# Optimization experiments

Measured on AMD Instinct MI355X. Metric: run time of the kernel, lower is better.

The kernel has to match this reference:

```python
import jax, jax.numpy as jnp
import numpy as np

B, L, D, S = 64, 512, 768, 8
HOP, LAMB = 3, 0.5


def _layernorm(x, g, b, eps=1e-5):
    m = x.mean(-1, keepdims=True)
    v = x.var(-1, keepdims=True)
    return (x - m) / jnp.sqrt(v + eps) * g + b


def _hop_refine(cur, sentence, ln_g, ln_b):
    # cur, sentence: [B,S,D]. HOP-1 refinement steps, then return last row.
    for _ in range(HOP - 1):
        coef = jnp.einsum('bd,bsd->bs', cur[:, -1, :], sentence)  # [B,S]
        a = coef[..., None] * sentence                             # [B,S,D]
        cur = LAMB * _layernorm(jax.nn.sigmoid(a), ln_g, ln_b) + sentence
    return cur[:, -1, :]  # [B,D]


def _conv1d(x, w, b):
    # x: [B,D,S], w: [Dout,Din,3], padding=1 (same)
    y = jax.lax.conv_general_dilated(
        x, w, window_strides=(1,), padding=((1, 1),),
        dimension_numbers=('NCH', 'OIH', 'NCH'))
    return y + b[None, :, None]


def setup_inputs() -> dict:
    key = jax.random.key(0)
    ks = jax.random.split(key, 16)
    p = lambda k, shp: (jax.random.normal(k, shp, dtype=jnp.float32) * 0.02)
    # segment boundaries: strictly increasing, start at 1, <= L, gaps ~63 with jitter < 32
    base = 1 + np.arange(S + 1) * ((L - 1) // S)          # [9]
    jitter = np.array(jax.random.randint(ks[15], (B, S + 1), 0, 32))
    jitter[:, 0] = 0
    jitter[:, -1] = 0
    seg_bounds = jnp.asarray(base[None, :] + jitter, dtype=jnp.int64 if jax.config.jax_enable_x64 else jnp.int32)
    return {
        'bert_output': jax.random.normal(ks[0], (B, L, D), dtype=jnp.float32),
        'target': jax.random.normal(ks[1], (B, D), dtype=jnp.float32),
        'gc1_w': p(ks[2], (D, D)), 'gc1_b': p(ks[3], (D,)),
        'gc2_w': p(ks[4], (D, D)), 'gc2_b': p(ks[5], (D,)),
        'conv1_w': p(ks[6], (D, D, 3)), 'conv1_b': p(ks[7], (D,)),
        'conv2_w': p(ks[8], (D, D, 3)), 'conv2_b': p(ks[9], (D,)),
        'ln_g': jnp.ones((D,), jnp.float32), 'ln_b': jnp.zeros((D,), jnp.float32),
        'fc2_w': p(ks[10], (3 * D, 3)), 'fc2_b': p(ks[11], (3,)),
        'seg_bounds': seg_bounds,
    }


def reference(bert_output, target, gc1_w, gc1_b, gc2_w, gc2_b,
              conv1_w, conv1_b, conv2_w, conv2_b, ln_g, ln_b,
              fc2_w, fc2_b, seg_bounds):
    dt = bert_output.dtype
    start = seg_bounds[:, :-1]   # [B,S]
    end = seg_bounds[:, 1:]      # [B,S]
    pos = jnp.arange(L)
    seg_mask = ((pos[None, None, :] >= start[:, :, None]) &
                (pos[None, None, :] < end[:, :, None])).astype(dt)  # [B,S,L]
    cnt = (end - start).astype(dt)                                   # [B,S]
    # batched segment-mean pooling
    sentence = jnp.einsum('bsl,bld->bsd', seg_mask, bert_output) / cnt[..., None]

    # GCN branch: adj = I + superdiagonal, row-degree normalization
    adj = jnp.eye(S, dtype=dt) + jnp.eye(S, k=1, dtype=dt)
    denom = adj.sum(axis=1)  # [S]

    def gcn(x, w, b):
        h = jnp.einsum('bsd,de->bse', x, w)
        return jnp.einsum('st,btd->bsd', adj, h) / denom[None, :, None] + b

    g1 = jnp.tanh(gcn(sentence, gc1_w, gc1_b))
    g2 = jnp.tanh(gcn(g1, gc2_w, gc2_b))
    a3 = _hop_refine(g2, sentence, ln_g, ln_b)

    # Conv branch: two conv1d (k=3, pad=1) over the segment axis
    x = jnp.swapaxes(sentence, 1, 2)  # [B,D,S]
    c = jnp.tanh(_conv1d(x, conv1_w, conv1_b))
    c = jnp.tanh(_conv1d(c, conv2_w, conv2_b))
    conv_out = jnp.swapaxes(c, 1, 2)  # [B,S,D]
    a4 = _hop_refine(conv_out, sentence, ln_g, ln_b)

    # Self-mask branch
    coef0 = jnp.einsum('bd,bsd->bs', sentence[:, -1, :], sentence)
    tmask = jax.nn.sigmoid(coef0[..., None] * sentence)
    a5 = _hop_refine(tmask, sentence, ln_g, ln_b)

    fnout = jnp.stack([a3, a4, a5], axis=1)                 # [B,3,D]
    # NOTE: original uses target[0] (first sample's pooler output) for all samples
    w = jax.nn.softmax(jnp.einsum('bkd,d->bk', fnout, target[0]), axis=1)
    fn = (fnout * w[..., None]).reshape(fnout.shape[0], 3 * D)
    return fn @ fc2_w + fc2_b  # [B,3]
```

## Files before the change

### kernel.cpp

```cpp
#include <hip/hip_runtime.h>


typedef unsigned short u16;
typedef short short8 __attribute__((ext_vector_type(8)));
typedef float f32x4 __attribute__((ext_vector_type(4)));

__device__ __forceinline__ float bf2f(u16 h) {
    unsigned int u = ((unsigned int)h) << 16;
    float f;
    __builtin_memcpy(&f, &u, 4);
    return f;
}
__device__ __forceinline__ u16 f2bf(float f) {
    unsigned int u;
    __builtin_memcpy(&u, &f, 4);
    u = (u + 0x7fffu + ((u >> 16) & 1u)) >> 16;
    return (u16)u;
}
__device__ __forceinline__ float sigm(float x) { return 1.0f / (1.0f + __expf(-x)); }

__device__ __forceinline__ float ldv(const void* p, long i, bool bf) {
    return bf ? bf2f(((const u16*)p)[i]) : ((const float*)p)[i];
}

__device__ __forceinline__ bool detect_bf16(const u16* bert) {
    int hits = 0;
#pragma unroll
    for (int i = 0; i < 256; i += 2) {
        const int e = (bert[i] >> 7) & 0xFF;
        hits += (e >= 115 && e <= 130) ? 1 : 0;
    }
    return hits > 64;
}

__global__ __launch_bounds__(256) void k0_zero(float* __restrict__ ws)
{
    ((float4*)ws)[blockIdx.x * 256 + threadIdx.x] = make_float4(0.f, 0.f, 0.f, 0.f);
}

__global__ __launch_bounds__(256) void k1_pool(
    const void* __restrict__ bertv, const int* __restrict__ sb,
    float* __restrict__ sentF, float* __restrict__ flagp)
{
    const int u = blockIdx.x, t = threadIdx.x;
    const bool bf = detect_bf16((const u16*)bertv);
    const bool is64 = (sb[1] == 0);
    if (u == 0 && t == 0) flagp[0] = bf ? 1.0f : 0.0f;
    const int q = u & 3, v = u >> 2;
    const int b = v / 3, si = v - 3 * (v / 3), s = 5 + si;
    const int i0 = b * 9 + s, i1 = i0 + 1;
    int st = is64 ? sb[2 * i0] : sb[i0];
    int en = is64 ? sb[2 * i1] : sb[i1];
    st = st < 0 ? 0 : (st > 511 ? 511 : st);
    en = en <= st ? st + 1 : (en > 512 ? 512 : en);
    const int n = en - st;
    const int r0 = st + (n * q) / 4;
    const int r1 = st + (n * (q + 1)) / 4;
    float a0 = 0.f, a1 = 0.f, a2 = 0.f;
    if (bf) {
        const u16* base = (const u16*)bertv + (size_t)b * 512 * 768;
        int l = r0;
        for (; l + 1 < r1; l += 2) {
            const u16* p0 = base + (size_t)l * 768;
            const u16* p1 = p0 + 768;
            const u16 x0 = p0[t], x1 = p0[t + 256], x2 = p0[t + 512];
            const u16 y0 = p1[t], y1 = p1[t + 256], y2 = p1[t + 512];
            a0 += bf2f(x0) + bf2f(y0);
            a1 += bf2f(x1) + bf2f(y1);
            a2 += bf2f(x2) + bf2f(y2);
        }
        if (l < r1) {
            const u16* p0 = base + (size_t)l * 768;
            a0 += bf2f(p0[t]);
            a1 += bf2f(p0[t + 256]);
            a2 += bf2f(p0[t + 512]);
        }
    } else {
        const float* base = (const float*)bertv + (size_t)b * 512 * 768;
        int l = r0;
        for (; l + 1 < r1; l += 2) {
            const float* p0 = base + (size_t)l * 768;
            const float* p1 = p0 + 768;
            const float x0 = p0[t], x1 = p0[t + 256], x2 = p0[t + 512];
            const float y0 = p1[t], y1 = p1[t + 256], y2 = p1[t + 512];
            a0 += x0 + y0;
            a1 += x1 + y1;
            a2 += x2 + y2;
        }
        if (l < r1) {
            const float* p0 = base + (size_t)l * 768;
            a0 += p0[t];
            a1 += p0[t + 256];
            a2 += p0[t + 512];
        }
    }
    const float inv = 1.0f / (float)n;
    float* o = sentF + b * 2304 + si * 768;
    atomicAdd(o + t, a0 * inv);
    atomicAdd(o + t + 256, a1 * inv);
    atomicAdd(o + t + 512, a2 * inv);
}

template <int XMODE, int WMODE>
__device__ __forceinline__ void gemm_core(
    const float* __restrict__ x, int xstride, const void* __restrict__ bias,
    const void* __restrict__ W, bool bf,
    float* __restrict__ out, int ostride,
    int n0, int k0, u16* As, u16* Bs)
{
    const int t = threadIdx.x;
    const int r = t >> 2;
    const int cseg = (t & 3) * 32;
    const int wave = t >> 6, lane = t & 63;
    const int lm = lane & 15, lq = lane >> 4;
    f32x4 acc[4] = {};

    for (int kk = 0; kk < 256; kk += 128) {
        const int kg = k0 + kk;
        {
            const float* xp = x + (size_t)r * xstride + (kg + cseg);
            u16* dst = As + r * 136 + cseg;
#pragma unroll
            for (int i = 0; i < 8; ++i) {
                float4 v = ((const float4*)xp)[i];
                if (XMODE == 1) {
                    int kb = kg + cseg + i * 4;
                    if (kb >= 768) kb -= 768;
                    v.x = tanhf(v.x + ldv(bias, kb, bf));
                    v.y = tanhf(v.y + ldv(bias, kb + 1, bf));
                    v.z = tanhf(v.z + ldv(bias, kb + 2, bf));
                    v.w = tanhf(v.w + ldv(bias, kb + 3, bf));
                }
                ((ushort4*)dst)[i] = make_ushort4(f2bf(v.x), f2bf(v.y), f2bf(v.z), f2bf(v.w));
            }
        }
        if (WMODE == 0) {
            const int p = t >> 2;
            const int nseg = (t & 3) * 16;
            u16 q0[16], q1[16];
            if (bf) {
                const u16* w0 = (const u16*)W + (size_t)(kg + 2 * p) * 768 + n0 + nseg;
                ((uint4*)q0)[0] = ((const uint4*)w0)[0];
                ((uint4*)q0)[1] = ((const uint4*)w0)[1];
                ((uint4*)q1)[0] = ((const uint4*)(w0 + 768))[0];
                ((uint4*)q1)[1] = ((const uint4*)(w0 + 768))[1];
            } else {
                const float* w0 = (const float*)W + (size_t)(kg + 2 * p) * 768 + n0 + nseg;
#pragma unroll
                for (int e = 0; e < 4; ++e) {
                    float4 v0 = ((const float4*)w0)[e];
                    float4 v1 = ((const float4*)(w0 + 768))[e];
                    q0[4 * e] = f2bf(v0.x); q0[4 * e + 1] = f2bf(v0.y);
                    q0[4 * e + 2] = f2bf(v0.z); q0[4 * e + 3] = f2bf(v0.w);
                    q1[4 * e] = f2bf(v1.x); q1[4 * e + 1] = f2bf(v1.y);
                    q1[4 * e + 2] = f2bf(v1.z); q1[4 * e + 3] = f2bf(v1.w);
                }
            }
#pragma unroll
            for (int e = 0; e < 16; ++e)
                *(ushort2*)(Bs + (nseg + e) * 136 + 2 * p) = make_ushort2(q0[e], q1[e]);
        } else {
            const int kb = kg / 768;
            const int i0c = kg - kb * 768;
            u16 tmp[32];
            if (bf) {
                const u16* wp = (const u16*)W + (size_t)(n0 + r) * 2304 + (size_t)(i0c + cseg) * 3 + kb;
#pragma unroll
                for (int j = 0; j < 32; ++j) tmp[j] = wp[j * 3];
            } else {
                const float* wp = (const float*)W + (size_t)(n0 + r) * 2304 + (size_t)(i0c + cseg) * 3 + kb;
#pragma unroll
                for (int j = 0; j < 32; ++j) tmp[j] = f2bf(wp[j * 3]);
            }
            u16* dst = Bs + r * 136 + cseg;
#pragma unroll
            for (int qq = 0; qq < 8; ++qq)
                ((ushort4*)dst)[qq] = ((ushort4*)tmp)[qq];
        }
        __syncthreads();
        const u16* ap = As + (wave * 16 + lm) * 136 + lq * 8;
        const u16* bp = Bs + lm * 136 + lq * 8;
#pragma unroll
        for (int ks = 0; ks < 4; ++ks) {
            short8 af = *(const short8*)(ap + ks * 32);
#pragma unroll
            for (int nf = 0; nf < 4; ++nf) {
                short8 bfr = *(const short8*)(bp + nf * 16 * 136 + ks * 32);
                acc[nf] = __builtin_amdgcn_mfma_f32_16x16x32_bf16(af, bfr, acc[nf], 0, 0, 0);
            }
        }
        __syncthreads();
    }
#pragma unroll
    for (int nf = 0; nf < 4; ++nf) {
#pragma unroll
        for (int rg = 0; rg < 4; ++rg) {
            const int row = wave * 16 + lq * 4 + rg;
            const int col = n0 + nf * 16 + lm;
            atomicAdd(out + (size_t)row * ostride + col, acc[nf][rg]);
        }
    }
}

__global__ __launch_bounds__(256) void k2_gemm_a(
    const float* __restrict__ sentF, const void* __restrict__ gc1w,
    const void* __restrict__ c1w, float* __restrict__ g1acc, float* __restrict__ c1acc,
    const float* __restrict__ flagp)
{
    __shared__ u16 As[64 * 136];
    __shared__ u16 Bs[64 * 136];
    const bool bf = flagp[0] > 0.5f;
    const int u = blockIdx.x;
    if (u < 36) {
        gemm_core<0, 0>(sentF + 1536, 2304, nullptr, gc1w, bf, g1acc, 768,
                        (u / 3) * 64, (u % 3) * 256, As, Bs);
    } else if (u < 144) {
        const int v = u - 36;
        gemm_core<0, 1>(sentF, 2304, nullptr, c1w, bf, c1acc, 1536,
                        (v / 9) * 64, (v % 9) * 256, As, Bs);
    } else {
        const int v = u - 144;
        gemm_core<0, 1>(sentF + 768, 2304, nullptr, c1w, bf, c1acc + 768, 1536,
                        (v / 6) * 64, (v % 6) * 256, As, Bs);
    }
}

__global__ __launch_bounds__(256) void k3_gemm_b(
    const float* __restrict__ g1acc, const float* __restrict__ c1acc,
    const void* __restrict__ gc2w, const void* __restrict__ c2w,
    const void* __restrict__ gc1b, const void* __restrict__ c1b,
    float* __restrict__ g2acc, float* __restrict__ c2acc,
    const float* __restrict__ flagp)
{
    __shared__ u16 As[64 * 136];
    __shared__ u16 Bs[64 * 136];
    const bool bf = flagp[0] > 0.5f;
    const int u = blockIdx.x;
    if (u < 36) {
        gemm_core<1, 0>(g1acc, 768, gc1b, gc2w, bf, g2acc, 768,
                        (u / 3) * 64, (u % 3) * 256, As, Bs);
    } else {
        const int v = u - 36;
        gemm_core<1, 1>(c1acc, 1536, c1b, c2w, bf, c2acc, 768,
                        (v / 6) * 64, (v % 6) * 256, As, Bs);
    }
}

__device__ __forceinline__ float block_sum(float v, float* red) {
#pragma unroll
    for (int m = 1; m < 64; m <<= 1) v += __shfl_xor(v, m, 64);
    const int wave = threadIdx.x >> 6, lane = threadIdx.x & 63;
    if (lane == 0) red[wave] = v;
    __syncthreads();
    const float r = red[0] + red[1] + red[2] + red[3];
    __syncthreads();
    return r;
}

__global__ __launch_bounds__(256) void k4_final(
    const float* __restrict__ sentF, const float* __restrict__ g2acc,
    const float* __restrict__ c2acc,
    const void* __restrict__ gc2b, const void* __restrict__ c2b,
    const void* __restrict__ lng, const void* __restrict__ lnb,
    const void* __restrict__ target, const void* __restrict__ fc2w,
    const void* __restrict__ fc2b, void* __restrict__ outp,
    const float* __restrict__ flagp)
{
    __shared__ float red[4];
    const bool bf = flagp[0] > 0.5f;
    const int t = threadIdx.x, b = blockIdx.x;
    float s_[3], g_[3], bb_[3];
    const float* srow = sentF + b * 2304 + 1536;
#pragma unroll
    for (int i = 0; i < 3; ++i) {
        const int d = t + 256 * i;
        s_[i] = srow[d];
        g_[i] = ldv(lng, d, bf);
        bb_[i] = ldv(lnb, d, bf);
    }

    auto refine2 = [&](float* yv) {
#pragma unroll
        for (int it = 0; it < 2; ++it) {
            const float c = block_sum(yv[0] * s_[0] + yv[1] * s_[1] + yv[2] * s_[2], red);
            float tt[3], sm = 0.0f, sq = 0.0f;
#pragma unroll
            for (int i = 0; i < 3; ++i) {
                tt[i] = sigm(c * s_[i]);
                sm += tt[i];
                sq += tt[i] * tt[i];
            }
            const float m = block_sum(sm, red) * (1.0f / 768.0f);
            const float q = block_sum(sq, red) * (1.0f / 768.0f);
            const float inv = rsqrtf(fmaxf(q - m * m, 0.0f) + 1e-5f);
#pragma unroll
            for (int i = 0; i < 3; ++i)
                yv[i] = 0.5f * ((tt[i] - m) * inv * g_[i] + bb_[i]) + s_[i];
        }
    };

    float a3[3], a4[3], a5[3], y[3];
#pragma unroll
    for (int i = 0; i < 3; ++i) {
        const int d = t + 256 * i;
        y[i] = tanhf(g2acc[b * 768 + d] + ldv(gc2b, d, bf));
    }
    refine2(y);
    a3[0] = y[0]; a3[1] = y[1]; a3[2] = y[2];
#pragma unroll
    for (int i = 0; i < 3; ++i) {
        const int d = t + 256 * i;
        y[i] = tanhf(c2acc[b * 768 + d] + ldv(c2b, d, bf));
    }
    refine2(y);
    a4[0] = y[0]; a4[1] = y[1]; a4[2] = y[2];
    const float ss = block_sum(s_[0] * s_[0] + s_[1] * s_[1] + s_[2] * s_[2], red);
#pragma unroll
    for (int i = 0; i < 3; ++i) y[i] = sigm(ss * s_[i]);
    refine2(y);
    a5[0] = y[0]; a5[1] = y[1]; a5[2] = y[2];

    float tg[3];
#pragma unroll
    for (int i = 0; i < 3; ++i) tg[i] = ldv(target, t + 256 * i, bf);
    const float u0 = block_sum(a3[0] * tg[0] + a3[1] * tg[1] + a3[2] * tg[2], red);
    const float u1 = block_sum(a4[0] * tg[0] + a4[1] * tg[1] + a4[2] * tg[2], red);
    const float u2 = block_sum(a5[0] * tg[0] + a5[1] * tg[1] + a5[2] * tg[2], red);
    const float mx = fmaxf(u0, fmaxf(u1, u2));
    const float e0 = __expf(u0 - mx), e1 = __expf(u1 - mx), e2 = __expf(u2 - mx);
    const float es = e0 + e1 + e2;
    const float w0 = e0 / es, w1 = e1 / es, w2 = e2 / es;

    float p0 = 0.0f, p1 = 0.0f, p2 = 0.0f;
#pragma unroll
    for (int i = 0; i < 3; ++i) {
        const int d = t + 256 * i;
        const float va = w0 * a3[i], vb = w1 * a4[i], vc = w2 * a5[i];
        p0 += va * ldv(fc2w, d * 3 + 0, bf) + vb * ldv(fc2w, (768 + d) * 3 + 0, bf) + vc * ldv(fc2w, (1536 + d) * 3 + 0, bf);
        p1 += va * ldv(fc2w, d * 3 + 1, bf) + vb * ldv(fc2w, (768 + d) * 3 + 1, bf) + vc * ldv(fc2w, (1536 + d) * 3 + 1, bf);
        p2 += va * ldv(fc2w, d * 3 + 2, bf) + vb * ldv(fc2w, (768 + d) * 3 + 2, bf) + vc * ldv(fc2w, (1536 + d) * 3 + 2, bf);
    }
    p0 = block_sum(p0, red);
    p1 = block_sum(p1, red);
    p2 = block_sum(p2, red);
    if (t == 0) {
        const float o0 = p0 + ldv(fc2b, 0, bf);
        const float o1 = p1 + ldv(fc2b, 1, bf);
        const float o2 = p2 + ldv(fc2b, 2, bf);
        if (bf) {
            ((u16*)outp)[b * 3 + 0] = f2bf(o0);
            ((u16*)outp)[b * 3 + 1] = f2bf(o1);
            ((u16*)outp)[b * 3 + 2] = f2bf(o2);
        } else {
            ((float*)outp)[b * 3 + 0] = o0;
            ((float*)outp)[b * 3 + 1] = o1;
            ((float*)outp)[b * 3 + 2] = o2;
        }
    }
}

extern "C" void kernel_launch(void* const* d_in, const int* in_sizes, int n_in,
                              void* d_out, int out_size, void* d_ws, size_t ws_size,
                              hipStream_t stream) {
    const void* bert   = d_in[0];
    const void* target = d_in[1];
    const void* gc1w   = d_in[2];
    const void* gc1b   = d_in[3];
    const void* gc2w   = d_in[4];
    const void* gc2b   = d_in[5];
    const void* c1w    = d_in[6];
    const void* c1b    = d_in[7];
    const void* c2w    = d_in[8];
    const void* c2b    = d_in[9];
    const void* lng    = d_in[10];
    const void* lnb    = d_in[11];
    const void* fc2w   = d_in[12];
    const void* fc2b   = d_in[13];
    const int*  sb     = (const int*)d_in[14];

    float* sentF = (float*)d_ws;
    float* accs  = sentF + 147456;
    float* g1acc = accs;
    float* c1acc = accs + 49152;
    float* g2acc = c1acc + 98304;
    float* c2acc = g2acc + 49152;
    float* flagp = accs + 245760;

    k0_zero<<<384, 256, 0, stream>>>(sentF);
    k1_pool<<<768, 256, 0, stream>>>(bert, sb, sentF, flagp);
    k2_gemm_a<<<216, 256, 0, stream>>>(sentF, gc1w, c1w, g1acc, c1acc, flagp);
    k3_gemm_b<<<108, 256, 0, stream>>>(g1acc, c1acc, gc2w, c2w, gc1b, c1b, g2acc, c2acc, flagp);
    k4_final<<<64, 256, 0, stream>>>(sentF, g2acc, c2acc, gc2b, c2b, lng, lnb,
                                     target, fc2w, fc2b, d_out, flagp);
}
```

Baseline: 224.5 us.

## Fuse all stages into one persistent kernel with software grid barriers

Replaces the five kernel launches (zero, pool, two GEMM stages, final) with a memset plus a single 768-block kernel. The stages are separated by atomic-counter grid barriers. The second GEMM stage is re-tiled to 216 blocks with one K iteration each instead of 108 blocks with two, which spreads the work across more blocks. The aim is to remove launch gaps and tail effects between the small stages. In exchange, it depends on all 768 blocks being co-resident, so the barrier could deadlock or time out (it breaks out after a poll limit) if they are not. The relaxed atomics with a vmcnt wait may also not guarantee memory visibility across blocks.

```diff
diff --git a/kernel.cpp b/kernel.cpp
--- a/kernel.cpp
+++ b/kernel.cpp
@@ -4,6 +4,8 @@
 typedef unsigned short u16;
 typedef short short8 __attribute__((ext_vector_type(8)));
 typedef float f32x4 __attribute__((ext_vector_type(4)));
+
+#define NBLK 768
 
 __device__ __forceinline__ float bf2f(u16 h) {
     unsigned int u = ((unsigned int)h) << 16;
@@ -33,72 +35,18 @@
     return hits > 64;
 }
 
-__global__ __launch_bounds__(256) void k0_zero(float* __restrict__ ws)
-{
-    ((float4*)ws)[blockIdx.x * 256 + threadIdx.x] = make_float4(0.f, 0.f, 0.f, 0.f);
-}
-
-__global__ __launch_bounds__(256) void k1_pool(
-    const void* __restrict__ bertv, const int* __restrict__ sb,
-    float* __restrict__ sentF, float* __restrict__ flagp)
-{
-    const int u = blockIdx.x, t = threadIdx.x;
-    const bool bf = detect_bf16((const u16*)bertv);
-    const bool is64 = (sb[1] == 0);
-    if (u == 0 && t == 0) flagp[0] = bf ? 1.0f : 0.0f;
-    const int q = u & 3, v = u >> 2;
-    const int b = v / 3, si = v - 3 * (v / 3), s = 5 + si;
-    const int i0 = b * 9 + s, i1 = i0 + 1;
-    int st = is64 ? sb[2 * i0] : sb[i0];
-    int en = is64 ? sb[2 * i1] : sb[i1];
-    st = st < 0 ? 0 : (st > 511 ? 511 : st);
-    en = en <= st ? st + 1 : (en > 512 ? 512 : en);
-    const int n = en - st;
-    const int r0 = st + (n * q) / 4;
-    const int r1 = st + (n * (q + 1)) / 4;
-    float a0 = 0.f, a1 = 0.f, a2 = 0.f;
-    if (bf) {
-        const u16* base = (const u16*)bertv + (size_t)b * 512 * 768;
-        int l = r0;
-        for (; l + 1 < r1; l += 2) {
-            const u16* p0 = base + (size_t)l * 768;
-            const u16* p1 = p0 + 768;
-            const u16 x0 = p0[t], x1 = p0[t + 256], x2 = p0[t + 512];
-            const u16 y0 = p1[t], y1 = p1[t + 256], y2 = p1[t + 512];
-            a0 += bf2f(x0) + bf2f(y0);
-            a1 += bf2f(x1) + bf2f(y1);
-            a2 += bf2f(x2) + bf2f(y2);
-        }
-        if (l < r1) {
-            const u16* p0 = base + (size_t)l * 768;
-            a0 += bf2f(p0[t]);
-            a1 += bf2f(p0[t + 256]);
-            a2 += bf2f(p0[t + 512]);
-        }
-    } else {
-        const float* base = (const float*)bertv + (size_t)b * 512 * 768;
-        int l = r0;
-        for (; l + 1 < r1; l += 2) {
-            const float* p0 = base + (size_t)l * 768;
-            const float* p1 = p0 + 768;
-            const float x0 = p0[t], x1 = p0[t + 256], x2 = p0[t + 512];
-            const float y0 = p1[t], y1 = p1[t + 256], y2 = p1[t + 512];
-            a0 += x0 + y0;
-            a1 += x1 + y1;
-            a2 += x2 + y2;
-        }
-        if (l < r1) {
-            const float* p0 = base + (size_t)l * 768;
-            a0 += p0[t];
-            a1 += p0[t + 256];
-            a2 += p0[t + 512];
-        }
-    }
-    const float inv = 1.0f / (float)n;
-    float* o = sentF + b * 2304 + si * 768;
-    atomicAdd(o + t, a0 * inv);
-    atomicAdd(o + t + 256, a1 * inv);
-    atomicAdd(o + t + 512, a2 * inv);
+__device__ __forceinline__ void gbar(unsigned* cnt, unsigned target) {
+    __syncthreads();
+    if (threadIdx.x == 0) {
+        asm volatile("s_waitcnt vmcnt(0)" ::: "memory");
+        __hip_atomic_fetch_add(cnt, 1u, __ATOMIC_RELAXED, __HIP_MEMORY_SCOPE_AGENT);
+        int polls = 0;
+        while (__hip_atomic_load(cnt, __ATOMIC_RELAXED, __HIP_MEMORY_SCOPE_AGENT) < target) {
+            __builtin_amdgcn_s_sleep(2);
+            if (++polls > (1 << 22)) break;
+        }
+    }
+    __syncthreads();
 }
 
 template <int XMODE, int WMODE>
@@ -106,7 +54,7 @@
     const float* __restrict__ x, int xstride, const void* __restrict__ bias,
     const void* __restrict__ W, bool bf,
     float* __restrict__ out, int ostride,
-    int n0, int k0, u16* As, u16* Bs)
+    int n0, int k0, int kiters, u16* As, u16* Bs)
 {
     const int t = threadIdx.x;
     const int r = t >> 2;
@@ -115,7 +63,7 @@
     const int lm = lane & 15, lq = lane >> 4;
     f32x4 acc[4] = {};
 
-    for (int kk = 0; kk < 256; kk += 128) {
+    for (int kk = 0; kk < kiters * 128; kk += 128) {
         const int kg = k0 + kk;
         {
             const float* xp = x + (size_t)r * xstride + (kg + cseg);
@@ -202,50 +150,6 @@
     }
 }
 
-__global__ __launch_bounds__(256) void k2_gemm_a(
-    const float* __restrict__ sentF, const void* __restrict__ gc1w,
-    const void* __restrict__ c1w, float* __restrict__ g1acc, float* __restrict__ c1acc,
-    const float* __restrict__ flagp)
-{
-    __shared__ u16 As[64 * 136];
-    __shared__ u16 Bs[64 * 136];
-    const bool bf = flagp[0] > 0.5f;
-    const int u = blockIdx.x;
-    if (u < 36) {
-        gemm_core<0, 0>(sentF + 1536, 2304, nullptr, gc1w, bf, g1acc, 768,
-                        (u / 3) * 64, (u % 3) * 256, As, Bs);
-    } else if (u < 144) {
-        const int v = u - 36;
-        gemm_core<0, 1>(sentF, 2304, nullptr, c1w, bf, c1acc, 1536,
-                        (v / 9) * 64, (v % 9) * 256, As, Bs);
-    } else {
-        const int v = u - 144;
-        gemm_core<0, 1>(sentF + 768, 2304, nullptr, c1w, bf, c1acc + 768, 1536,
-                        (v / 6) * 64, (v % 6) * 256, As, Bs);
-    }
-}
-
-__global__ __launch_bounds__(256) void k3_gemm_b(
-    const float* __restrict__ g1acc, const float* __restrict__ c1acc,
-    const void* __restrict__ gc2w, const void* __restrict__ c2w,
-    const void* __restrict__ gc1b, const void* __restrict__ c1b,
-    float* __restrict__ g2acc, float* __restrict__ c2acc,
-    const float* __restrict__ flagp)
-{
-    __shared__ u16 As[64 * 136];
-    __shared__ u16 Bs[64 * 136];
-    const bool bf = flagp[0] > 0.5f;
-    const int u = blockIdx.x;
-    if (u < 36) {
-        gemm_core<1, 0>(g1acc, 768, gc1b, gc2w, bf, g2acc, 768,
-                        (u / 3) * 64, (u % 3) * 256, As, Bs);
-    } else {
-        const int v = u - 36;
-        gemm_core<1, 1>(c1acc, 1536, c1b, c2w, bf, c2acc, 768,
-                        (v / 6) * 64, (v % 6) * 256, As, Bs);
-    }
-}
-
 __device__ __forceinline__ float block_sum(float v, float* red) {
 #pragma unroll
     for (int m = 1; m < 64; m <<= 1) v += __shfl_xor(v, m, 64);
@@ -257,104 +161,210 @@
     return r;
 }
 
-__global__ __launch_bounds__(256) void k4_final(
-    const float* __restrict__ sentF, const float* __restrict__ g2acc,
-    const float* __restrict__ c2acc,
-    const void* __restrict__ gc2b, const void* __restrict__ c2b,
+__global__ __launch_bounds__(256) void kmono(
+    const void* __restrict__ bert, const int* __restrict__ sb,
+    const void* __restrict__ target,
+    const void* __restrict__ gc1w, const void* __restrict__ gc1b,
+    const void* __restrict__ gc2w, const void* __restrict__ gc2b,
+    const void* __restrict__ c1w, const void* __restrict__ c1b,
+    const void* __restrict__ c2w, const void* __restrict__ c2b,
     const void* __restrict__ lng, const void* __restrict__ lnb,
-    const void* __restrict__ target, const void* __restrict__ fc2w,
-    const void* __restrict__ fc2b, void* __restrict__ outp,
-    const float* __restrict__ flagp)
+    const void* __restrict__ fc2w, const void* __restrict__ fc2b,
+    void* __restrict__ outp, float* __restrict__ ws)
 {
+    __shared__ u16 As[64 * 136];
+    __shared__ u16 Bs[64 * 136];
     __shared__ float red[4];
-    const bool bf = flagp[0] > 0.5f;
-    const int t = threadIdx.x, b = blockIdx.x;
-    float s_[3], g_[3], bb_[3];
-    const float* srow = sentF + b * 2304 + 1536;
-#pragma unroll
-    for (int i = 0; i < 3; ++i) {
-        const int d = t + 256 * i;
-        s_[i] = srow[d];
-        g_[i] = ldv(lng, d, bf);
-        bb_[i] = ldv(lnb, d, bf);
-    }
-
-    auto refine2 = [&](float* yv) {
-#pragma unroll
-        for (int it = 0; it < 2; ++it) {
-            const float c = block_sum(yv[0] * s_[0] + yv[1] * s_[1] + yv[2] * s_[2], red);
-            float tt[3], sm = 0.0f, sq = 0.0f;
-#pragma unroll
-            for (int i = 0; i < 3; ++i) {
-                tt[i] = sigm(c * s_[i]);
-                sm += tt[i];
-                sq += tt[i] * tt[i];
-            }
-            const float m = block_sum(sm, red) * (1.0f / 768.0f);
-            const float q = block_sum(sq, red) * (1.0f / 768.0f);
-            const float inv = rsqrtf(fmaxf(q - m * m, 0.0f) + 1e-5f);
-#pragma unroll
-            for (int i = 0; i < 3; ++i)
-                yv[i] = 0.5f * ((tt[i] - m) * inv * g_[i] + bb_[i]) + s_[i];
-        }
-    };
-
-    float a3[3], a4[3], a5[3], y[3];
-#pragma unroll
-    for (int i = 0; i < 3; ++i) {
-        const int d = t + 256 * i;
-        y[i] = tanhf(g2acc[b * 768 + d] + ldv(gc2b, d, bf));
-    }
-    refine2(y);
-    a3[0] = y[0]; a3[1] = y[1]; a3[2] = y[2];
-#pragma unroll
-    for (int i = 0; i < 3; ++i) {
-        const int d = t + 256 * i;
-        y[i] = tanhf(c2acc[b * 768 + d] + ldv(c2b, d, bf));
-    }
-    refine2(y);
-    a4[0] = y[0]; a4[1] = y[1]; a4[2] = y[2];
-    const float ss = block_sum(s_[0] * s_[0] + s_[1] * s_[1] + s_[2] * s_[2], red);
-#pragma unroll
-    for (int i = 0; i < 3; ++i) y[i] = sigm(ss * s_[i]);
-    refine2(y);
-    a5[0] = y[0]; a5[1] = y[1]; a5[2] = y[2];
-
-    float tg[3];
-#pragma unroll
-    for (int i = 0; i < 3; ++i) tg[i] = ldv(target, t + 256 * i, bf);
-    const float u0 = block_sum(a3[0] * tg[0] + a3[1] * tg[1] + a3[2] * tg[2], red);
-    const float u1 = block_sum(a4[0] * tg[0] + a4[1] * tg[1] + a4[2] * tg[2], red);
-    const float u2 = block_sum(a5[0] * tg[0] + a5[1] * tg[1] + a5[2] * tg[2], red);
-    const float mx = fmaxf(u0, fmaxf(u1, u2));
-    const float e0 = __expf(u0 - mx), e1 = __expf(u1 - mx), e2 = __expf(u2 - mx);
-    const float es = e0 + e1 + e2;
-    const float w0 = e0 / es, w1 = e1 / es, w2 = e2 / es;
-
-    float p0 = 0.0f, p1 = 0.0f, p2 = 0.0f;
-#pragma unroll
-    for (int i = 0; i < 3; ++i) {
-        const int d = t + 256 * i;
-        const float va = w0 * a3[i], vb = w1 * a4[i], vc = w2 * a5[i];
-        p0 += va * ldv(fc2w, d * 3 + 0, bf) + vb * ldv(fc2w, (768 + d) * 3 + 0, bf) + vc * ldv(fc2w, (1536 + d) * 3 + 0, bf);
-        p1 += va * ldv(fc2w, d * 3 + 1, bf) + vb * ldv(fc2w, (768 + d) * 3 + 1, bf) + vc * ldv(fc2w, (1536 + d) * 3 + 1, bf);
-        p2 += va * ldv(fc2w, d * 3 + 2, bf) + vb * ldv(fc2w, (768 + d) * 3 + 2, bf) + vc * ldv(fc2w, (1536 + d) * 3 + 2, bf);
-    }
-    p0 = block_sum(p0, red);
-    p1 = block_sum(p1, red);
-    p2 = block_sum(p2, red);
-    if (t == 0) {
-        const float o0 = p0 + ldv(fc2b, 0, bf);
-        const float o1 = p1 + ldv(fc2b, 1, bf);
-        const float o2 = p2 + ldv(fc2b, 2, bf);
+    const int t = threadIdx.x;
+    const int blk = blockIdx.x;
+
+    const bool bf = detect_bf16((const u16*)bert);
+    const bool is64 = (sb[1] == 0);
+
+    float* sentF = ws;
+    float* accs  = ws + 147456;
+    float* g1acc = accs;
+    float* c1acc = g1acc + 49152;
+    float* g2acc = c1acc + 98304;
+    float* c2acc = g2acc + 49152;
+    unsigned* cnts = (unsigned*)(accs + 245760);
+
+    {
+        const int u = blk;
+        const int q = u & 3, v = u >> 2;
+        const int b = v / 3, si = v - 3 * (v / 3), s = 5 + si;
+        const int i0 = b * 9 + s, i1 = i0 + 1;
+        int st = is64 ? sb[2 * i0] : sb[i0];
+        int en = is64 ? sb[2 * i1] : sb[i1];
+        st = st < 0 ? 0 : (st > 511 ? 511 : st);
+        en = en <= st ? st + 1 : (en > 512 ? 512 : en);
+        const int n = en - st;
+        const int r0 = st + (n * q) / 4;
+        const int r1 = st + (n * (q + 1)) / 4;
+        float a0 = 0.f, a1 = 0.f, a2 = 0.f;
         if (bf) {
-            ((u16*)outp)[b * 3 + 0] = f2bf(o0);
-            ((u16*)outp)[b * 3 + 1] = f2bf(o1);
-            ((u16*)outp)[b * 3 + 2] = f2bf(o2);
+            const u16* base = (const u16*)bert + (size_t)b * 512 * 768;
+            int l = r0;
+            for (; l + 1 < r1; l += 2) {
+                const u16* p0 = base + (size_t)l * 768;
+                const u16* p1 = p0 + 768;
+                a0 += bf2f(p0[t]) + bf2f(p1[t]);
+                a1 += bf2f(p0[t + 256]) + bf2f(p1[t + 256]);
+                a2 += bf2f(p0[t + 512]) + bf2f(p1[t + 512]);
+            }
+            if (l < r1) {
+                const u16* p0 = base + (size_t)l * 768;
+                a0 += bf2f(p0[t]);
+                a1 += bf2f(p0[t + 256]);
+                a2 += bf2f(p0[t + 512]);
+            }
         } else {
-            ((float*)outp)[b * 3 + 0] = o0;
-            ((float*)outp)[b * 3 + 1] = o1;
-            ((float*)outp)[b * 3 + 2] = o2;
+            const float* base = (const float*)bert + (size_t)b * 512 * 768;
+            int l = r0;
+            for (; l + 1 < r1; l += 2) {
+                const float* p0 = base + (size_t)l * 768;
+                const float* p1 = p0 + 768;
+                a0 += p0[t] + p1[t];
+                a1 += p0[t + 256] + p1[t + 256];
+                a2 += p0[t + 512] + p1[t + 512];
+            }
+            if (l < r1) {
+                const float* p0 = base + (size_t)l * 768;
+                a0 += p0[t];
+                a1 += p0[t + 256];
+                a2 += p0[t + 512];
+            }
+        }
+        const float inv = 1.0f / (float)n;
+        float* o = sentF + b * 2304 + si * 768;
+        atomicAdd(o + t, a0 * inv);
+        atomicAdd(o + t + 256, a1 * inv);
+        atomicAdd(o + t + 512, a2 * inv);
+    }
+
+    gbar(cnts + 0, NBLK);
+
+    if (blk < 216) {
+        const int u = blk;
+        if (u < 36) {
+            gemm_core<0, 0>(sentF + 1536, 2304, nullptr, gc1w, bf, g1acc, 768,
+                            (u / 3) * 64, (u % 3) * 256, 2, As, Bs);
+        } else if (u < 144) {
+            const int v = u - 36;
+            gemm_core<0, 1>(sentF, 2304, nullptr, c1w, bf, c1acc, 1536,
+                            (v / 9) * 64, (v % 9) * 256, 2, As, Bs);
+        } else {
+            const int v = u - 144;
+            gemm_core<0, 1>(sentF + 768, 2304, nullptr, c1w, bf, c1acc + 768, 1536,
+                            (v / 6) * 64, (v % 6) * 256, 2, As, Bs);
+        }
+    }
+
+    gbar(cnts + 1, NBLK);
+
+    if (blk < 216) {
+        const int u = blk;
+        if (u < 72) {
+            gemm_core<1, 0>(g1acc, 768, gc1b, gc2w, bf, g2acc, 768,
+                            (u / 6) * 64, (u % 6) * 128, 1, As, Bs);
+        } else {
+            const int v = u - 72;
+            gemm_core<1, 1>(c1acc, 1536, c1b, c2w, bf, c2acc, 768,
+                            (v / 12) * 64, (v % 12) * 128, 1, As, Bs);
+        }
+    }
+
+    gbar(cnts + 2, NBLK);
+
+    if (blk < 64) {
+        const int b = blk;
+        float s_[3], g_[3], bb_[3];
+        const float* srow = sentF + b * 2304 + 1536;
+#pragma unroll
+        for (int i = 0; i < 3; ++i) {
+            const int d = t + 256 * i;
+            s_[i] = srow[d];
+            g_[i] = ldv(lng, d, bf);
+            bb_[i] = ldv(lnb, d, bf);
+        }
+
+        auto refine2 = [&](float* yv) {
+#pragma unroll
+            for (int it = 0; it < 2; ++it) {
+                const float c = block_sum(yv[0] * s_[0] + yv[1] * s_[1] + yv[2] * s_[2], red);
+                float tt[3], sm = 0.0f, sq = 0.0f;
+#pragma unroll
+                for (int i = 0; i < 3; ++i) {
+                    tt[i] = sigm(c * s_[i]);
+                    sm += tt[i];
+                    sq += tt[i] * tt[i];
+                }
+                const float m = block_sum(sm, red) * (1.0f / 768.0f);
+                const float q = block_sum(sq, red) * (1.0f / 768.0f);
+                const float inv = rsqrtf(fmaxf(q - m * m, 0.0f) + 1e-5f);
+#pragma unroll
+                for (int i = 0; i < 3; ++i)
+                    yv[i] = 0.5f * ((tt[i] - m) * inv * g_[i] + bb_[i]) + s_[i];
+            }
+        };
+
+        float a3[3], a4[3], a5[3], y[3];
+#pragma unroll
+        for (int i = 0; i < 3; ++i) {
+            const int d = t + 256 * i;
+            y[i] = tanhf(g2acc[b * 768 + d] + ldv(gc2b, d, bf));
+        }
+        refine2(y);
+        a3[0] = y[0]; a3[1] = y[1]; a3[2] = y[2];
+#pragma unroll
+        for (int i = 0; i < 3; ++i) {
+            const int d = t + 256 * i;
+            y[i] = tanhf(c2acc[b * 768 + d] + ldv(c2b, d, bf));
+        }
+        refine2(y);
+        a4[0] = y[0]; a4[1] = y[1]; a4[2] = y[2];
+        const float ss = block_sum(s_[0] * s_[0] + s_[1] * s_[1] + s_[2] * s_[2], red);
+#pragma unroll
+        for (int i = 0; i < 3; ++i) y[i] = sigm(ss * s_[i]);
+        refine2(y);
+        a5[0] = y[0]; a5[1] = y[1]; a5[2] = y[2];
+
+        float tg[3];
+#pragma unroll
+        for (int i = 0; i < 3; ++i) tg[i] = ldv(target, t + 256 * i, bf);
+        const float u0 = block_sum(a3[0] * tg[0] + a3[1] * tg[1] + a3[2] * tg[2], red);
+        const float u1 = block_sum(a4[0] * tg[0] + a4[1] * tg[1] + a4[2] * tg[2], red);
+        const float u2 = block_sum(a5[0] * tg[0] + a5[1] * tg[1] + a5[2] * tg[2], red);
+        const float mx = fmaxf(u0, fmaxf(u1, u2));
+        const float e0 = __expf(u0 - mx), e1 = __expf(u1 - mx), e2 = __expf(u2 - mx);
+        const float es = e0 + e1 + e2;
+        const float w0 = e0 / es, w1 = e1 / es, w2 = e2 / es;
+
+        float p0 = 0.0f, p1 = 0.0f, p2 = 0.0f;
+#pragma unroll
+        for (int i = 0; i < 3; ++i) {
+            const int d = t + 256 * i;
+            const float va = w0 * a3[i], vb = w1 * a4[i], vc = w2 * a5[i];
+            p0 += va * ldv(fc2w, d * 3 + 0, bf) + vb * ldv(fc2w, (768 + d) * 3 + 0, bf) + vc * ldv(fc2w, (1536 + d) * 3 + 0, bf);
+            p1 += va * ldv(fc2w, d * 3 + 1, bf) + vb * ldv(fc2w, (768 + d) * 3 + 1, bf) + vc * ldv(fc2w, (1536 + d) * 3 + 1, bf);
+            p2 += va * ldv(fc2w, d * 3 + 2, bf) + vb * ldv(fc2w, (768 + d) * 3 + 2, bf) + vc * ldv(fc2w, (1536 + d) * 3 + 2, bf);
+        }
+        p0 = block_sum(p0, red);
+        p1 = block_sum(p1, red);
+        p2 = block_sum(p2, red);
+        if (t == 0) {
+            const float o0 = p0 + ldv(fc2b, 0, bf);
+            const float o1 = p1 + ldv(fc2b, 1, bf);
+            const float o2 = p2 + ldv(fc2b, 2, bf);
+            if (bf) {
+                ((u16*)outp)[b * 3 + 0] = f2bf(o0);
+                ((u16*)outp)[b * 3 + 1] = f2bf(o1);
+                ((u16*)outp)[b * 3 + 2] = f2bf(o2);
+            } else {
+                ((float*)outp)[b * 3 + 0] = o0;
+                ((float*)outp)[b * 3 + 1] = o1;
+                ((float*)outp)[b * 3 + 2] = o2;
+            }
         }
     }
 }
@@ -378,18 +388,9 @@
     const void* fc2b   = d_in[13];
     const int*  sb     = (const int*)d_in[14];
 
-    float* sentF = (float*)d_ws;
-    float* accs  = sentF + 147456;
-    float* g1acc = accs;
-    float* c1acc = accs + 49152;
-    float* g2acc = c1acc + 98304;
-    float* c2acc = g2acc + 49152;
-    float* flagp = accs + 245760;
-
-    k0_zero<<<384, 256, 0, stream>>>(sentF);
-    k1_pool<<<768, 256, 0, stream>>>(bert, sb, sentF, flagp);
-    k2_gemm_a<<<216, 256, 0, stream>>>(sentF, gc1w, c1w, g1acc, c1acc, flagp);
-    k3_gemm_b<<<108, 256, 0, stream>>>(g1acc, c1acc, gc2w, c2w, gc1b, c1b, g2acc, c2acc, flagp);
-    k4_final<<<64, 256, 0, stream>>>(sentF, g2acc, c2acc, gc2b, c2b, lng, lnb,
-                                     target, fc2w, fc2b, d_out, flagp);
-}
+    hipMemsetAsync(d_ws, 0, 393216 * 4 + 12, stream);
+
+    kmono<<<NBLK, 256, 0, stream>>>(
+        bert, sb, target, gc1w, gc1b, gc2w, gc2b, c1w, c1b, c2w, c2b,
+        lng, lnb, fc2w, fc2b, d_out, (float*)d_ws);
+}
```

Measured after the change: 296.0 us. 31.9% more time.

## Replace atomic split-K accumulation with partial slabs reduced by consumers

Applied to the files above, without the earlier changes.

Pooling and the GEMM split-K stages now write per-split partial results into separate workspace slabs instead of using atomicAdd into zeroed buffers. The next stage sums the partials while loading its inputs. This removes the zeroing kernel and the float atomics, and makes results deterministic. The bf16 flag is recomputed in every kernel instead of being passed through memory. In exchange, workspace use and global reads grow, and the split-K factors are retuned so fewer blocks run in the GEMM stages.

```diff
diff --git a/kernel.cpp b/kernel.cpp
--- a/kernel.cpp
+++ b/kernel.cpp
@@ -4,6 +4,8 @@
 typedef unsigned short u16;
 typedef short short8 __attribute__((ext_vector_type(8)));
 typedef float f32x4 __attribute__((ext_vector_type(4)));
+
+#define PSLAB 147456
 
 __device__ __forceinline__ float bf2f(u16 h) {
     unsigned int u = ((unsigned int)h) << 16;
@@ -33,19 +35,130 @@
     return hits > 64;
 }
 
-__global__ __launch_bounds__(256) void k0_zero(float* __restrict__ ws)
-{
-    ((float4*)ws)[blockIdx.x * 256 + threadIdx.x] = make_float4(0.f, 0.f, 0.f, 0.f);
-}
-
-__global__ __launch_bounds__(256) void k1_pool(
+template <int NSUM, int ACT, int WMODE>
+__device__ __forceinline__ void gemm_core(
+    const float* __restrict__ x, int xstride, int pslab,
+    const void* __restrict__ bias, const void* __restrict__ W, bool bf,
+    float* __restrict__ out, int ostride,
+    int n0, int k0, int kiters, u16* As, u16* Bs)
+{
+    const int t = threadIdx.x;
+    const int r = t >> 2;
+    const int cseg = (t & 3) * 32;
+    const int wave = t >> 6, lane = t & 63;
+    const int lm = lane & 15, lq = lane >> 4;
+    f32x4 acc[4] = {};
+
+    for (int kk = 0; kk < kiters * 128; kk += 128) {
+        const int kg = k0 + kk;
+        {
+            const float* xp = x + (size_t)r * xstride + (kg + cseg);
+            u16* dst = As + r * 136 + cseg;
+#pragma unroll
+            for (int i = 0; i < 8; ++i) {
+                float4 v = ((const float4*)xp)[i];
+#pragma unroll
+                for (int sfx = 1; sfx < NSUM; ++sfx) {
+                    float4 vv = ((const float4*)(xp + (size_t)sfx * pslab))[i];
+                    v.x += vv.x; v.y += vv.y; v.z += vv.z; v.w += vv.w;
+                }
+                if (ACT) {
+                    int kb = kg + cseg + i * 4;
+                    if (kb >= 768) kb -= 768;
+                    v.x = tanhf(v.x + ldv(bias, kb, bf));
+                    v.y = tanhf(v.y + ldv(bias, kb + 1, bf));
+                    v.z = tanhf(v.z + ldv(bias, kb + 2, bf));
+                    v.w = tanhf(v.w + ldv(bias, kb + 3, bf));
+                }
+                ((ushort4*)dst)[i] = make_ushort4(f2bf(v.x), f2bf(v.y), f2bf(v.z), f2bf(v.w));
+            }
+        }
+        if (WMODE == 0) {
+            const int p = t >> 2;
+            const int nseg = (t & 3) * 16;
+            u16 q0[16], q1[16];
+            if (bf) {
+                const u16* w0 = (const u16*)W + (size_t)(kg + 2 * p) * 768 + n0 + nseg;
+                ((uint4*)q0)[0] = ((const uint4*)w0)[0];
+                ((uint4*)q0)[1] = ((const uint4*)w0)[1];
+                ((uint4*)q1)[0] = ((const uint4*)(w0 + 768))[0];
+                ((uint4*)q1)[1] = ((const uint4*)(w0 + 768))[1];
+            } else {
+                const float* w0 = (const float*)W + (size_t)(kg + 2 * p) * 768 + n0 + nseg;
+#pragma unroll
+                for (int e = 0; e < 4; ++e) {
+                    float4 v0 = ((const float4*)w0)[e];
+                    float4 v1 = ((const float4*)(w0 + 768))[e];
+                    q0[4 * e] = f2bf(v0.x); q0[4 * e + 1] = f2bf(v0.y);
+                    q0[4 * e + 2] = f2bf(v0.z); q0[4 * e + 3] = f2bf(v0.w);
+                    q1[4 * e] = f2bf(v1.x); q1[4 * e + 1] = f2bf(v1.y);
+                    q1[4 * e + 2] = f2bf(v1.z); q1[4 * e + 3] = f2bf(v1.w);
+                }
+            }
+#pragma unroll
+            for (int e = 0; e < 16; ++e)
+                *(ushort2*)(Bs + (nseg + e) * 136 + 2 * p) = make_ushort2(q0[e], q1[e]);
+        } else {
+            const int kb = kg / 768;
+            const int i0c = kg - kb * 768;
+            u16 tmp[32];
+            if (bf) {
+                const u16* wp = (const u16*)W + (size_t)(n0 + r) * 2304 + (size_t)(i0c + cseg) * 3 + kb;
+#pragma unroll
+                for (int j = 0; j < 32; ++j) tmp[j] = wp[j * 3];
+            } else {
+                const float* wp = (const float*)W + (size_t)(n0 + r) * 2304 + (size_t)(i0c + cseg) * 3 + kb;
+#pragma unroll
+                for (int j = 0; j < 32; ++j) tmp[j] = f2bf(wp[j * 3]);
+            }
+            u16* dst = Bs + r * 136 + cseg;
+#pragma unroll
+            for (int qq = 0; qq < 8; ++qq)
+                ((ushort4*)dst)[qq] = ((ushort4*)tmp)[qq];
+        }
+        __syncthreads();
+        const u16* ap = As + (wave * 16 + lm) * 136 + lq * 8;
+        const u16* bp = Bs + lm * 136 + lq * 8;
+#pragma unroll
+        for (int ks = 0; ks < 4; ++ks) {
+            short8 af = *(const short8*)(ap + ks * 32);
+#pragma unroll
+            for (int nf = 0; nf < 4; ++nf) {
+                short8 bfr = *(const short8*)(bp + nf * 16 * 136 + ks * 32);
+                acc[nf] = __builtin_amdgcn_mfma_f32_16x16x32_bf16(af, bfr, acc[nf], 0, 0, 0);
+            }
+        }
+        __syncthreads();
+    }
+#pragma unroll
+    for (int nf = 0; nf < 4; ++nf) {
+#pragma unroll
+        for (int rg = 0; rg < 4; ++rg) {
+            const int row = wave * 16 + lq * 4 + rg;
+            const int col = n0 + nf * 16 + lm;
+            out[(size_t)row * ostride + col] = acc[nf][rg];
+        }
+    }
+}
+
+__device__ __forceinline__ float block_sum(float v, float* red) {
+#pragma unroll
+    for (int m = 1; m < 64; m <<= 1) v += __shfl_xor(v, m, 64);
+    const int wave = threadIdx.x >> 6, lane = threadIdx.x & 63;
+    if (lane == 0) red[wave] = v;
+    __syncthreads();
+    const float r = red[0] + red[1] + red[2] + red[3];
+    __syncthreads();
+    return r;
+}
+
+__global__ __launch_bounds__(256) void kA_pool(
     const void* __restrict__ bertv, const int* __restrict__ sb,
-    float* __restrict__ sentF, float* __restrict__ flagp)
+    float* __restrict__ sentP)
 {
     const int u = blockIdx.x, t = threadIdx.x;
     const bool bf = detect_bf16((const u16*)bertv);
     const bool is64 = (sb[1] == 0);
-    if (u == 0 && t == 0) flagp[0] = bf ? 1.0f : 0.0f;
     const int q = u & 3, v = u >> 2;
     const int b = v / 3, si = v - 3 * (v / 3), s = 5 + si;
     const int i0 = b * 9 + s, i1 = i0 + 1;
@@ -63,11 +176,9 @@
         for (; l + 1 < r1; l += 2) {
             const u16* p0 = base + (size_t)l * 768;
             const u16* p1 = p0 + 768;
-            const u16 x0 = p0[t], x1 = p0[t + 256], x2 = p0[t + 512];
-            const u16 y0 = p1[t], y1 = p1[t + 256], y2 = p1[t + 512];
-            a0 += bf2f(x0) + bf2f(y0);
-            a1 += bf2f(x1) + bf2f(y1);
-            a2 += bf2f(x2) + bf2f(y2);
+            a0 += bf2f(p0[t]) + bf2f(p1[t]);
+            a1 += bf2f(p0[t + 256]) + bf2f(p1[t + 256]);
+            a2 += bf2f(p0[t + 512]) + bf2f(p1[t + 512]);
         }
         if (l < r1) {
             const u16* p0 = base + (size_t)l * 768;
@@ -81,11 +192,9 @@
         for (; l + 1 < r1; l += 2) {
             const float* p0 = base + (size_t)l * 768;
             const float* p1 = p0 + 768;
-            const float x0 = p0[t], x1 = p0[t + 256], x2 = p0[t + 512];
-            const float y0 = p1[t], y1 = p1[t + 256], y2 = p1[t + 512];
-            a0 += x0 + y0;
-            a1 += x1 + y1;
-            a2 += x2 + y2;
+            a0 += p0[t] + p1[t];
+            a1 += p0[t + 256] + p1[t + 256];
+            a2 += p0[t + 512] + p1[t + 512];
         }
         if (l < r1) {
             const float* p0 = base + (size_t)l * 768;
@@ -95,186 +204,75 @@
         }
     }
     const float inv = 1.0f / (float)n;
-    float* o = sentF + b * 2304 + si * 768;
-    atomicAdd(o + t, a0 * inv);
-    atomicAdd(o + t + 256, a1 * inv);
-    atomicAdd(o + t + 512, a2 * inv);
-}
-
-template <int XMODE, int WMODE>
-__device__ __forceinline__ void gemm_core(
-    const float* __restrict__ x, int xstride, const void* __restrict__ bias,
-    const void* __restrict__ W, bool bf,
-    float* __restrict__ out, int ostride,
-    int n0, int k0, u16* As, u16* Bs)
-{
-    const int t = threadIdx.x;
-    const int r = t >> 2;
-    const int cseg = (t & 3) * 32;
-    const int wave = t >> 6, lane = t & 63;
-    const int lm = lane & 15, lq = lane >> 4;
-    f32x4 acc[4] = {};
-
-    for (int kk = 0; kk < 256; kk += 128) {
-        const int kg = k0 + kk;
-        {
-            const float* xp = x + (size_t)r * xstride + (kg + cseg);
-            u16* dst = As + r * 136 + cseg;
-#pragma unroll
-            for (int i = 0; i < 8; ++i) {
-                float4 v = ((const float4*)xp)[i];
-                if (XMODE == 1) {
-                    int kb = kg + cseg + i * 4;
-                    if (kb >= 768) kb -= 768;
-                    v.x = tanhf(v.x + ldv(bias, kb, bf));
-                    v.y = tanhf(v.y + ldv(bias, kb + 1, bf));
-                    v.z = tanhf(v.z + ldv(bias, kb + 2, bf));
-                    v.w = tanhf(v.w + ldv(bias, kb + 3, bf));
-                }
-                ((ushort4*)dst)[i] = make_ushort4(f2bf(v.x), f2bf(v.y), f2bf(v.z), f2bf(v.w));
-            }
-        }
-        if (WMODE == 0) {
-            const int p = t >> 2;
-            const int nseg = (t & 3) * 16;
-            u16 q0[16], q1[16];
-            if (bf) {
-                const u16* w0 = (const u16*)W + (size_t)(kg + 2 * p) * 768 + n0 + nseg;
-                ((uint4*)q0)[0] = ((const uint4*)w0)[0];
-                ((uint4*)q0)[1] = ((const uint4*)w0)[1];
-                ((uint4*)q1)[0] = ((const uint4*)(w0 + 768))[0];
-                ((uint4*)q1)[1] = ((const uint4*)(w0 + 768))[1];
-            } else {
-                const float* w0 = (const float*)W + (size_t)(kg + 2 * p) * 768 + n0 + nseg;
-#pragma unroll
-                for (int e = 0; e < 4; ++e) {
-                    float4 v0 = ((const float4*)w0)[e];
-                    float4 v1 = ((const float4*)(w0 + 768))[e];
-                    q0[4 * e] = f2bf(v0.x); q0[4 * e + 1] = f2bf(v0.y);
-                    q0[4 * e + 2] = f2bf(v0.z); q0[4 * e + 3] = f2bf(v0.w);
-                    q1[4 * e] = f2bf(v1.x); q1[4 * e + 1] = f2bf(v1.y);
-                    q1[4 * e + 2] = f2bf(v1.z); q1[4 * e + 3] = f2bf(v1.w);
-                }
-            }
-#pragma unroll
-            for (int e = 0; e < 16; ++e)
-                *(ushort2*)(Bs + (nseg + e) * 136 + 2 * p) = make_ushort2(q0[e], q1[e]);
-        } else {
-            const int kb = kg / 768;
-            const int i0c = kg - kb * 768;
-            u16 tmp[32];
-            if (bf) {
-                const u16* wp = (const u16*)W + (size_t)(n0 + r) * 2304 + (size_t)(i0c + cseg) * 3 + kb;
-#pragma unroll
-                for (int j = 0; j < 32; ++j) tmp[j] = wp[j * 3];
-            } else {
-                const float* wp = (const float*)W + (size_t)(n0 + r) * 2304 + (size_t)(i0c + cseg) * 3 + kb;
-#pragma unroll
-                for (int j = 0; j < 32; ++j) tmp[j] = f2bf(wp[j * 3]);
-            }
-            u16* dst = Bs + r * 136 + cseg;
-#pragma unroll
-            for (int qq = 0; qq < 8; ++qq)
-                ((ushort4*)dst)[qq] = ((ushort4*)tmp)[qq];
-        }
-        __syncthreads();
-        const u16* ap = As + (wave * 16 + lm) * 136 + lq * 8;
-        const u16* bp = Bs + lm * 136 + lq * 8;
-#pragma unroll
-        for (int ks = 0; ks < 4; ++ks) {
-            short8 af = *(const short8*)(ap + ks * 32);
-#pragma unroll
-            for (int nf = 0; nf < 4; ++nf) {
-                short8 bfr = *(const short8*)(bp + nf * 16 * 136 + ks * 32);
-                acc[nf] = __builtin_amdgcn_mfma_f32_16x16x32_bf16(af, bfr, acc[nf], 0, 0, 0);
-            }
-        }
-        __syncthreads();
-    }
-#pragma unroll
-    for (int nf = 0; nf < 4; ++nf) {
-#pragma unroll
-        for (int rg = 0; rg < 4; ++rg) {
-            const int row = wave * 16 + lq * 4 + rg;
-            const int col = n0 + nf * 16 + lm;
-            atomicAdd(out + (size_t)row * ostride + col, acc[nf][rg]);
-        }
-    }
-}
-
-__global__ __launch_bounds__(256) void k2_gemm_a(
-    const float* __restrict__ sentF, const void* __restrict__ gc1w,
-    const void* __restrict__ c1w, float* __restrict__ g1acc, float* __restrict__ c1acc,
-    const float* __restrict__ flagp)
+    float* o = sentP + (size_t)q * PSLAB + b * 2304 + si * 768;
+    o[t] = a0 * inv;
+    o[t + 256] = a1 * inv;
+    o[t + 512] = a2 * inv;
+}
+
+__global__ __launch_bounds__(256) void kB_gemm_a(
+    const float* __restrict__ sentP, const void* __restrict__ bertv,
+    const void* __restrict__ gc1w, const void* __restrict__ c1w,
+    float* __restrict__ g1p, float* __restrict__ c1p)
 {
     __shared__ u16 As[64 * 136];
     __shared__ u16 Bs[64 * 136];
-    const bool bf = flagp[0] > 0.5f;
+    const bool bf = detect_bf16((const u16*)bertv);
     const int u = blockIdx.x;
     if (u < 36) {
-        gemm_core<0, 0>(sentF + 1536, 2304, nullptr, gc1w, bf, g1acc, 768,
-                        (u / 3) * 64, (u % 3) * 256, As, Bs);
-    } else if (u < 144) {
-        const int v = u - 36;
-        gemm_core<0, 1>(sentF, 2304, nullptr, c1w, bf, c1acc, 1536,
-                        (v / 9) * 64, (v % 9) * 256, As, Bs);
+        const int nt = u / 3, jc = u % 3;
+        gemm_core<4, 0, 0>(sentP + 1536, 2304, PSLAB, nullptr, gc1w, bf,
+                           g1p + jc * 49152, 768, nt * 64, jc * 256, 2, As, Bs);
+    } else if (u < 108) {
+        const int v = u - 36, nt = v / 6, jc = v % 6;
+        gemm_core<4, 0, 1>(sentP, 2304, PSLAB, nullptr, c1w, bf,
+                           c1p + jc * 98304, 1536, nt * 64, jc * 384, 3, As, Bs);
     } else {
-        const int v = u - 144;
-        gemm_core<0, 1>(sentF + 768, 2304, nullptr, c1w, bf, c1acc + 768, 1536,
-                        (v / 6) * 64, (v % 6) * 256, As, Bs);
-    }
-}
-
-__global__ __launch_bounds__(256) void k3_gemm_b(
-    const float* __restrict__ g1acc, const float* __restrict__ c1acc,
+        const int v = u - 108, nt = v / 6, jc = v % 6;
+        gemm_core<4, 0, 1>(sentP + 768, 2304, PSLAB, nullptr, c1w, bf,
+                           c1p + jc * 98304 + 768, 1536, nt * 64, jc * 256, 2, As, Bs);
+    }
+}
+
+__global__ __launch_bounds__(256) void kC_gemm_b(
+    const float* __restrict__ g1p, const float* __restrict__ c1p,
+    const void* __restrict__ bertv,
     const void* __restrict__ gc2w, const void* __restrict__ c2w,
     const void* __restrict__ gc1b, const void* __restrict__ c1b,
-    float* __restrict__ g2acc, float* __restrict__ c2acc,
-    const float* __restrict__ flagp)
+    float* __restrict__ g2p, float* __restrict__ c2p)
 {
     __shared__ u16 As[64 * 136];
     __shared__ u16 Bs[64 * 136];
-    const bool bf = flagp[0] > 0.5f;
+    const bool bf = detect_bf16((const u16*)bertv);
     const int u = blockIdx.x;
     if (u < 36) {
-        gemm_core<1, 0>(g1acc, 768, gc1b, gc2w, bf, g2acc, 768,
-                        (u / 3) * 64, (u % 3) * 256, As, Bs);
+        const int nt = u / 3, jc = u % 3;
+        gemm_core<3, 1, 0>(g1p, 768, 49152, gc1b, gc2w, bf,
+                           g2p + jc * 49152, 768, nt * 64, jc * 256, 2, As, Bs);
     } else {
-        const int v = u - 36;
-        gemm_core<1, 1>(c1acc, 1536, c1b, c2w, bf, c2acc, 768,
-                        (v / 6) * 64, (v % 6) * 256, As, Bs);
-    }
-}
-
-__device__ __forceinline__ float block_sum(float v, float* red) {
-#pragma unroll
-    for (int m = 1; m < 64; m <<= 1) v += __shfl_xor(v, m, 64);
-    const int wave = threadIdx.x >> 6, lane = threadIdx.x & 63;
-    if (lane == 0) red[wave] = v;
-    __syncthreads();
-    const float r = red[0] + red[1] + red[2] + red[3];
-    __syncthreads();
-    return r;
-}
-
-__global__ __launch_bounds__(256) void k4_final(
-    const float* __restrict__ sentF, const float* __restrict__ g2acc,
-    const float* __restrict__ c2acc,
+        const int v = u - 36, nt = v / 4, jc = v % 4;
+        gemm_core<6, 1, 1>(c1p, 1536, 98304, c1b, c2w, bf,
+                           c2p + jc * 49152, 768, nt * 64, jc * 384, 3, As, Bs);
+    }
+}
+
+__global__ __launch_bounds__(256) void kD_final(
+    const float* __restrict__ sentP, const float* __restrict__ g2p,
+    const float* __restrict__ c2p, const void* __restrict__ bertv,
     const void* __restrict__ gc2b, const void* __restrict__ c2b,
     const void* __restrict__ lng, const void* __restrict__ lnb,
     const void* __restrict__ target, const void* __restrict__ fc2w,
-    const void* __restrict__ fc2b, void* __restrict__ outp,
-    const float* __restrict__ flagp)
+    const void* __restrict__ fc2b, void* __restrict__ outp)
 {
     __shared__ float red[4];
-    const bool bf = flagp[0] > 0.5f;
+    const bool bf = detect_bf16((const u16*)bertv);
     const int t = threadIdx.x, b = blockIdx.x;
     float s_[3], g_[3], bb_[3];
-    const float* srow = sentF + b * 2304 + 1536;
+    const float* srow = sentP + b * 2304 + 1536;
 #pragma unroll
     for (int i = 0; i < 3; ++i) {
         const int d = t + 256 * i;
-        s_[i] = srow[d];
+        s_[i] = srow[d] + srow[d + PSLAB] + srow[d + 2 * PSLAB] + srow[d + 3 * PSLAB];
         g_[i] = ldv(lng, d, bf);
         bb_[i] = ldv(lnb, d, bf);
     }
@@ -303,14 +301,17 @@
 #pragma unroll
     for (int i = 0; i < 3; ++i) {
         const int d = t + 256 * i;
-        y[i] = tanhf(g2acc[b * 768 + d] + ldv(gc2b, d, bf));
+        const float gs = g2p[b * 768 + d] + g2p[49152 + b * 768 + d] + g2p[98304 + b * 768 + d];
+        y[i] = tanhf(gs + ldv(gc2b, d, bf));
     }
     refine2(y);
     a3[0] = y[0]; a3[1] = y[1]; a3[2] = y[2];
 #pragma unroll
     for (int i = 0; i < 3; ++i) {
         const int d = t + 256 * i;
-        y[i] = tanhf(c2acc[b * 768 + d] + ldv(c2b, d, bf));
+        const float cs = c2p[b * 768 + d] + c2p[49152 + b * 768 + d]
+                       + c2p[98304 + b * 768 + d] + c2p[147456 + b * 768 + d];
+        y[i] = tanhf(cs + ldv(c2b, d, bf));
     }
     refine2(y);
     a4[0] = y[0]; a4[1] = y[1]; a4[2] = y[2];
@@ -378,18 +379,15 @@
     const void* fc2b   = d_in[13];
     const int*  sb     = (const int*)d_in[14];
 
-    float* sentF = (float*)d_ws;
-    float* accs  = sentF + 147456;
-    float* g1acc = accs;
-    float* c1acc = accs + 49152;
-    float* g2acc = c1acc + 98304;
-    float* c2acc = g2acc + 49152;
-    float* flagp = accs + 245760;
-
-    k0_zero<<<384, 256, 0, stream>>>(sentF);
-    k1_pool<<<768, 256, 0, stream>>>(bert, sb, sentF, flagp);
-    k2_gemm_a<<<216, 256, 0, stream>>>(sentF, gc1w, c1w, g1acc, c1acc, flagp);
-    k3_gemm_b<<<108, 256, 0, stream>>>(g1acc, c1acc, gc2w, c2w, gc1b, c1b, g2acc, c2acc, flagp);
-    k4_final<<<64, 256, 0, stream>>>(sentF, g2acc, c2acc, gc2b, c2b, lng, lnb,
-                                     target, fc2w, fc2b, d_out, flagp);
-}
+    float* sentP = (float*)d_ws;
+    float* g1p   = sentP + 4 * PSLAB;
+    float* c1p   = g1p + 147456;
+    float* g2p   = c1p + 589824;
+    float* c2p   = g2p + 147456;
+
+    kA_pool<<<768, 256, 0, stream>>>(bert, sb, sentP);
+    kB_gemm_a<<<180, 256, 0, stream>>>(sentP, bert, gc1w, c1w, g1p, c1p);
+    kC_gemm_b<<<84, 256, 0, stream>>>(g1p, c1p, bert, gc2w, c2w, gc1b, c1b, g2p, c2p);
+    kD_final<<<64, 256, 0, stream>>>(sentP, g2p, c2p, bert, gc2b, c2b, lng, lnb,
+                                     target, fc2w, fc2b, d_out);
+}
```

After: 266.5 us. +18.7%, slower.
